# Kernel tuning notes

Hardware: AMD Instinct MI355X
Metric: run time of the kernel (lower is better)

The kernel has to match this reference:

```python
import jax, jax.numpy as jnp
import numpy as np

P = 64       # number of pathways
NV = 512     # features per pathway (nvar[i])
W = 256      # hidden width per pathway
COV = 16     # covariates
B = 2048     # batch
EPS = 1e-5   # BatchNorm eps
SLOPE = 0.2  # LeakyReLU negative slope


def _lrelu(v):
    return jnp.where(v >= 0, v, SLOPE * v)


def setup_inputs() -> dict:
    key = jax.random.key(0)
    ks = jax.random.split(key, 8)
    x = jax.random.normal(ks[0], (B, P * NV + COV), dtype=jnp.float32)
    # per-pathway weights (no bias), stacked across pathways -> grouped GEMM
    W1 = jax.random.normal(ks[1], (P, NV, W), dtype=jnp.float32) * (1.0 / np.sqrt(NV))
    W2 = jax.random.normal(ks[2], (P, W, W), dtype=jnp.float32) * (1.0 / np.sqrt(W))
    W3 = jax.random.normal(ks[3], (P, W), dtype=jnp.float32) * (1.0 / np.sqrt(W))
    gamma = jnp.ones((P,), dtype=jnp.float32)   # bn_path weight
    beta = jnp.zeros((P,), dtype=jnp.float32)   # bn_path bias
    fc_w = jax.random.normal(ks[4], (P + COV, 1), dtype=jnp.float32) * 0.05
    fc_b = jnp.full((1,), 0.001, dtype=jnp.float32)
    return {"x": x, "W1": W1, "W2": W2, "W3": W3,
            "gamma": gamma, "beta": beta, "fc_w": fc_w, "fc_b": fc_b}


def reference(x, W1, W2, W3, gamma, beta, fc_w, fc_b):
    # pathway blocks (dropout = identity in eval): grouped GEMMs over P pathways
    xp = x[:, : P * NV].reshape(B, P, NV)
    h = _lrelu(jnp.einsum('bpi,pio->bpo', xp, W1))
    h = _lrelu(jnp.einsum('bpi,pio->bpo', h, W2))
    p = _lrelu(jnp.einsum('bpi,pi->bp', h, W3))          # [B, P]
    # BatchNorm1d (training-mode batch statistics, biased variance)
    mean = p.mean(axis=0)
    var = p.var(axis=0)
    pn = (p - mean) / jnp.sqrt(var + EPS) * gamma + beta
    # global L2 (Frobenius) normalization, as torch.norm(pathway_layer, 2)
    pn = pn / jnp.linalg.norm(pn)
    # concat covariates, final linear + sigmoid
    z = jnp.concatenate([pn, x[:, P * NV: P * NV + COV]], axis=1)  # [B, P+COV]
    return jax.nn.sigmoid(z @ fc_w + fc_b)                         # [B, 1]
```

## Files before the change

### kernel.cpp

```cpp
#include <hip/hip_runtime.h>
#include <hip/hip_bf16.h>

#define PW 64
#define NV 512
#define HW 256
#define COV 16
#define BATCH 2048
#define XROW (PW * NV + COV)
#define IMG 16384
#define IMG2 8192

typedef short s16x8 __attribute__((ext_vector_type(8)));
typedef float f32x4 __attribute__((ext_vector_type(4)));

__device__ __forceinline__ unsigned short f2bf(float f) {
    union { float f; unsigned int u; } v;
    v.f = f;
    unsigned int u = v.u;
    unsigned int r = (u + 0x7fffu + ((u >> 16) & 1u)) >> 16;
    return (unsigned short)r;
}

__device__ __forceinline__ unsigned int pack2(float a, float b) {
    __hip_bfloat162 h = __float22bfloat162_rn(float2{a, b});
    union { __hip_bfloat162 h; unsigned int u; } c;
    c.h = h;
    return c.u;
}

__device__ __forceinline__ float lrelu(float v) { return v >= 0.f ? v : 0.2f * v; }

__device__ __forceinline__ void gl_lds16(const void* g, void* l) {
    __builtin_amdgcn_global_load_lds(
        (const __attribute__((address_space(1))) void*)g,
        (__attribute__((address_space(3))) void*)l, 16, 0, 0);
}

#define WAITV(n) asm volatile("s_waitcnt vmcnt(" #n ") lgkmcnt(0)" ::: "memory")
#define BAR()    __builtin_amdgcn_s_barrier()
#define SCHED0() __builtin_amdgcn_sched_barrier(0)

__global__ __launch_bounds__(256)
void transpose_all(const float* __restrict__ W1, const float* __restrict__ W2,
                   unsigned short* __restrict__ W1I, unsigned short* __restrict__ W2I) {
    __shared__ float tile[64][260];
    int bx = blockIdx.x;
    const int t = threadIdx.x;
    const bool isW1 = bx < 512;
    const float* src;
    if (isW1) {
        int p = bx >> 3, kb = bx & 7;
        src = W1 + ((size_t)p * NV + kb * 64) * HW;
    } else {
        int b2 = bx - 512;
        int p = b2 >> 2, kb64 = b2 & 3;
        src = W2 + ((size_t)p * HW + kb64 * 64) * HW;
    }
    #pragma unroll
    for (int i = 0; i < 16; ++i) {
        int idx = t + i * 256;
        int r = idx >> 6, c4 = (idx & 63) << 2;
        *(float4*)&tile[r][c4] = *(const float4*)(src + (size_t)r * HW + c4);
    }
    __syncthreads();
    if (isW1) {
        int p = bx >> 3, kb = bx & 7;
        unsigned short* dst = W1I + (size_t)(p * 8 + kb) * IMG;
        #pragma unroll
        for (int pass = 0; pass < 8; ++pass) {
            int idx = pass * 256 + t;
            int n = idx >> 3, s = idx & 7;
            int g = s ^ (n & 7);
            unsigned short v[8];
            #pragma unroll
            for (int j = 0; j < 8; ++j)
                v[j] = f2bf(tile[g * 8 + j][n]);
            *(s16x8*)(dst + (size_t)idx * 8) = *(s16x8*)v;
        }
    } else {
        int b2 = bx - 512;
        int p = b2 >> 2, kb64 = b2 & 3;
        unsigned short* dst = W2I + (size_t)(p * 8 + kb64 * 2) * IMG2;
        #pragma unroll
        for (int pass = 0; pass < 8; ++pass) {
            int idx = pass * 256 + t;
            int h = idx >> 10;
            int rem = idx & 1023;
            int n = rem >> 2, s = rem & 3;
            int g = s ^ ((n >> 1) & 3);
            int krow = h * 32 + g * 8;
            unsigned short v[8];
            #pragma unroll
            for (int j = 0; j < 8; ++j)
                v[j] = f2bf(tile[krow + j][n]);
            *(s16x8*)(dst + (size_t)h * IMG2 + n * 32 + s * 8) = *(s16x8*)v;
        }
    }
}

__global__ __launch_bounds__(512, 2)
void pathway_fused(const float* __restrict__ x, const unsigned short* __restrict__ W1I,
                   const unsigned short* __restrict__ W2I, const float* __restrict__ W3,
                   float* __restrict__ pvec) {
    __shared__ __align__(16) unsigned short lds[81920];

    const int lin = blockIdx.x;
    const int xcd = lin & 7;
    const int idx = lin >> 3;
    const int p   = xcd * 8 + (idx >> 3);
    const int mt  = idx & 7;
    const int bm0 = mt * 256;

    const int t = threadIdx.x;
    const int lane = t & 63;
    const int wave = t >> 6;
    const int wm   = wave >> 2;
    const int wn   = wave & 3;
    const int l15  = lane & 15;
    const int quad = lane >> 4;

    const float* Ap          = x   + (size_t)p * NV;
    const unsigned short* B1 = W1I + (size_t)p * 8 * IMG;
    const unsigned short* B2 = W2I + (size_t)p * 8 * IMG2;

    int arow[8], acolc[8], aoff[8];
    #pragma unroll
    for (int i = 0; i < 8; ++i) {
        int ii = t + i * 512;
        arow[i]  = ii >> 4;
        acolc[i] = (ii & 15) * 4;
        int slot = (acolc[i] >> 3) ^ (arow[i] & 7);
        aoff[i]  = arow[i] * 64 + slot * 8 + (acolc[i] & 7);
    }

    float4 S[8];
    f32x4 acc[8][4] = {};

#define XLOAD(k0) { \
    _Pragma("unroll") \
    for (int i = 0; i < 8; ++i) \
        S[i] = *(const float4*)(Ap + (size_t)(bm0 + arow[i]) * XROW + (k0) + acolc[i]); }

#define APACK(buf) { \
    unsigned short* Asb = lds + (buf) * 16384; \
    _Pragma("unroll") \
    for (int i = 0; i < 8; ++i) { \
        uint2 u; \
        u.x = pack2(S[i].x, S[i].y); \
        u.y = pack2(S[i].z, S[i].w); \
        *(uint2*)&Asb[aoff[i]] = u; } }

#define B1STAGE(buf, kb) { \
    const unsigned short* img = B1 + (size_t)(kb) * IMG; \
    _Pragma("unroll") \
    for (int c = 0; c < 4; ++c) { \
        int off = wave * 4096 + c * 1024; \
        gl_lds16((const char*)img + off + lane * 16, \
                 (char*)lds + 65536 + (buf) * 32768 + off); } }

#define MFMA_A(buf) { \
    const unsigned short* Asb = lds + (buf) * 16384; \
    const unsigned short* Bsb = lds + 32768 + (buf) * 16384; \
    __builtin_amdgcn_s_setprio(1); \
    _Pragma("unroll") \
    for (int kk = 0; kk < 64; kk += 32) { \
        s16x8 af[8], bfr[4]; \
        _Pragma("unroll") \
        for (int mi = 0; mi < 8; ++mi) { \
            int row = wm * 128 + mi * 16 + l15; \
            int slot = ((kk >> 3) + quad) ^ (row & 7); \
            af[mi] = *(const s16x8*)&Asb[row * 64 + slot * 8]; } \
        _Pragma("unroll") \
        for (int ni = 0; ni < 4; ++ni) { \
            int row = wn * 64 + ni * 16 + l15; \
            int slot = ((kk >> 3) + quad) ^ (row & 7); \
            bfr[ni] = *(const s16x8*)&Bsb[row * 64 + slot * 8]; } \
        _Pragma("unroll") \
        for (int mi = 0; mi < 8; ++mi) \
            _Pragma("unroll") \
            for (int ni = 0; ni < 4; ++ni) \
                acc[mi][ni] = __builtin_amdgcn_mfma_f32_16x16x32_bf16( \
                    af[mi], bfr[ni], acc[mi][ni], 0, 0, 0); } \
    __builtin_amdgcn_s_setprio(0); }

#define W2STAGE(buf, kb) { \
    const unsigned short* img = B2 + (size_t)(kb) * IMG2; \
    _Pragma("unroll") \
    for (int c = 0; c < 2; ++c) { \
        int off = wave * 2048 + c * 1024; \
        gl_lds16((const char*)img + off + lane * 16, \
                 (char*)lds + 131072 + (buf) * 16384 + off); } }

#define MFMA_B(buf, kb) { \
    const unsigned short* W2b = lds + 65536 + (buf) * 8192; \
    __builtin_amdgcn_s_setprio(1); \
    { \
        s16x8 af[8], bfr[4]; \
        _Pragma("unroll") \
        for (int mi = 0; mi < 8; ++mi) { \
            int row = wm * 128 + mi * 16 + l15; \
            int slot = ((kb) * 4 + quad) ^ (row & 7); \
            af[mi] = *(const s16x8*)&lds[row * 256 + slot * 8]; } \
        _Pragma("unroll") \
        for (int ni = 0; ni < 4; ++ni) { \
            int row = wn * 64 + ni * 16 + l15; \
            int slot = quad ^ ((row >> 1) & 3); \
            bfr[ni] = *(const s16x8*)&W2b[row * 32 + slot * 8]; } \
        _Pragma("unroll") \
        for (int mi = 0; mi < 8; ++mi) \
            _Pragma("unroll") \
            for (int ni = 0; ni < 4; ++ni) \
                acc[mi][ni] = __builtin_amdgcn_mfma_f32_16x16x32_bf16( \
                    af[mi], bfr[ni], acc[mi][ni], 0, 0, 0); \
    } \
    __builtin_amdgcn_s_setprio(0); }

#define STEP_A(tt, WN) { \
    if ((tt) + 1 < 8) B1STAGE(1 - ((tt) & 1), (tt) + 1); \
    SCHED0(); \
    if ((tt) + 1 < 8) APACK(1 - ((tt) & 1)); \
    if ((tt) + 2 < 8) XLOAD(((tt) + 2) * 64); \
    SCHED0(); \
    MFMA_A((tt) & 1); \
    WAITV(WN); \
    BAR(); \
    SCHED0(); }

#define STEP_B(tt) { \
    if ((tt) + 1 < 8) W2STAGE(1 - ((tt) & 1), (tt) + 1); \
    SCHED0(); \
    MFMA_B((tt) & 1, (tt)); \
    WAITV(0); \
    BAR(); \
    SCHED0(); }

    XLOAD(0);
    SCHED0();
    B1STAGE(0, 0);
    SCHED0();
    APACK(0);
    XLOAD(64);
    WAITV(8);
    BAR();
    SCHED0();

    STEP_A(0, 8);
    STEP_A(1, 8);
    STEP_A(2, 8);
    STEP_A(3, 8);
    STEP_A(4, 8);
    STEP_A(5, 8);
    STEP_A(6, 0);
    STEP_A(7, 0);

    W2STAGE(0, 0);
    SCHED0();
    #pragma unroll
    for (int mi = 0; mi < 8; ++mi)
        #pragma unroll
        for (int ni = 0; ni < 4; ++ni)
            #pragma unroll
            for (int r = 0; r < 4; ++r) {
                int row = wm * 128 + mi * 16 + quad * 4 + r;
                int col = wn * 64 + ni * 16 + l15;
                int slot = (col >> 3) ^ (row & 7);
                lds[row * 256 + slot * 8 + (col & 7)] = f2bf(lrelu(acc[mi][ni][r]));
            }
    WAITV(0);
    BAR();
    SCHED0();

    #pragma unroll
    for (int mi = 0; mi < 8; ++mi)
        #pragma unroll
        for (int ni = 0; ni < 4; ++ni)
            acc[mi][ni] = (f32x4){0.f, 0.f, 0.f, 0.f};

    STEP_B(0);
    STEP_B(1);
    STEP_B(2);
    STEP_B(3);
    STEP_B(4);
    STEP_B(5);
    STEP_B(6);
    STEP_B(7);

    float* red = (float*)lds;
    float w3v[4];
    #pragma unroll
    for (int ni = 0; ni < 4; ++ni)
        w3v[ni] = W3[(size_t)p * HW + wn * 64 + ni * 16 + l15];
    float part[8][4];
    #pragma unroll
    for (int mi = 0; mi < 8; ++mi) {
        #pragma unroll
        for (int r = 0; r < 4; ++r) {
            float s = 0.f;
            #pragma unroll
            for (int ni = 0; ni < 4; ++ni)
                s += lrelu(acc[mi][ni][r]) * w3v[ni];
            part[mi][r] = s;
        }
    }
    #pragma unroll
    for (int off = 1; off < 16; off <<= 1)
        #pragma unroll
        for (int mi = 0; mi < 8; ++mi)
            #pragma unroll
            for (int r = 0; r < 4; ++r)
                part[mi][r] += __shfl_xor(part[mi][r], off);
    if (l15 == 0)
        #pragma unroll
        for (int mi = 0; mi < 8; ++mi)
            #pragma unroll
            for (int r = 0; r < 4; ++r)
                red[wn * 256 + wm * 128 + mi * 16 + quad * 4 + r] = part[mi][r];
    __syncthreads();
    if (t < 256) {
        float s = red[0 * 256 + t] + red[1 * 256 + t] + red[2 * 256 + t] + red[3 * 256 + t];
        pvec[(size_t)p * BATCH + bm0 + t] = lrelu(s);
    }
#undef XLOAD
#undef APACK
#undef B1STAGE
#undef MFMA_A
#undef W2STAGE
#undef MFMA_B
#undef STEP_A
#undef STEP_B
}

__global__ __launch_bounds__(256)
void stats_k(const float* __restrict__ pvec, float* __restrict__ stat) {
    const int p = blockIdx.x;
    float s = 0.f, q = 0.f;
    for (int i = threadIdx.x; i < BATCH; i += 256) {
        float v = pvec[(size_t)p * BATCH + i];
        s += v; q += v * v;
    }
    #pragma unroll
    for (int off = 32; off; off >>= 1) {
        s += __shfl_down(s, off);
        q += __shfl_down(q, off);
    }
    __shared__ float ls[4], lq[4];
    const int wave = threadIdx.x >> 6, lane = threadIdx.x & 63;
    if (lane == 0) { ls[wave] = s; lq[wave] = q; }
    __syncthreads();
    if (threadIdx.x == 0) {
        float S = ls[0] + ls[1] + ls[2] + ls[3];
        float Q = lq[0] + lq[1] + lq[2] + lq[3];
        float mean = S * (1.f / BATCH);
        float var  = Q * (1.f / BATCH) - mean * mean;
        stat[p]       = mean;
        stat[64 + p]  = rsqrtf(var + 1e-5f);
        stat[128 + p] = var;
    }
}

__global__ __launch_bounds__(256)
void final_k(const float* __restrict__ pvec, const float* __restrict__ stat,
             const float* __restrict__ gamma, const float* __restrict__ beta,
             const float* __restrict__ x, const float* __restrict__ fc_w,
             const float* __restrict__ fc_b, float* __restrict__ out) {
    const int b = blockIdx.x * 256 + threadIdx.x;
    float nsq = 0.f;
    #pragma unroll
    for (int p = 0; p < PW; ++p) {
        float g = gamma[p], bt = beta[p], var = stat[128 + p], inv = stat[64 + p];
        nsq += (float)BATCH * (g * g * var * inv * inv + bt * bt);
    }
    const float rn = rsqrtf(nsq);
    float acc = fc_b[0];
    #pragma unroll
    for (int p = 0; p < PW; ++p) {
        float pn = (pvec[(size_t)p * BATCH + b] - stat[p]) * stat[64 + p] * gamma[p] + beta[p];
        acc += pn * rn * fc_w[p];
    }
    #pragma unroll
    for (int c = 0; c < COV; ++c)
        acc += x[(size_t)b * XROW + PW * NV + c] * fc_w[PW + c];
    out[b] = 1.f / (1.f + __expf(-acc));
}

extern "C" void kernel_launch(void* const* d_in, const int* in_sizes, int n_in,
                              void* d_out, int out_size, void* d_ws, size_t ws_size,
                              hipStream_t stream) {
    const float* x     = (const float*)d_in[0];
    const float* W1    = (const float*)d_in[1];
    const float* W2    = (const float*)d_in[2];
    const float* W3    = (const float*)d_in[3];
    const float* gamma = (const float*)d_in[4];
    const float* beta  = (const float*)d_in[5];
    const float* fc_w  = (const float*)d_in[6];
    const float* fc_b  = (const float*)d_in[7];
    float* out = (float*)d_out;

    char* ws = (char*)d_ws;
    size_t off = 0;
    unsigned short* W1I = (unsigned short*)(ws + off); off += (size_t)PW * NV * HW * 2;
    unsigned short* W2I = (unsigned short*)(ws + off); off += (size_t)PW * HW * HW * 2;
    float* pvec = (float*)(ws + off); off += (size_t)PW * BATCH * 4;
    float* stat = (float*)(ws + off); off += 256 * 4;

    transpose_all<<<dim3(512 + 256), 256, 0, stream>>>(W1, W2, W1I, W2I);
    pathway_fused<<<dim3(512), 512, 0, stream>>>(x, W1I, W2I, W3, pvec);
    stats_k<<<PW, 256, 0, stream>>>(pvec, stat);
    final_k<<<BATCH / 256, 256, 0, stream>>>(pvec, stat, gamma, beta, x, fc_w, fc_b, out);
}
```

Baseline: 455.8 us.

## Triple-buffer W1 staging in GEMM1 and fuse batch statistics into pathway kernel

Reworks the first GEMM loop so W1 tiles are staged into three LDS buffers two steps ahead, and moves the X pack after the MFMA block so loads overlap compute more deeply. It also folds the per-pathway sum and sum-of-squares reduction into the fused kernel's epilogue using atomics. This removes the separate stats kernel launch and its re-read of pvec. The atomics are zeroed inside the transpose kernel, which adds a dependency, and float atomic ordering makes the statistics nondeterministic.

```diff
diff --git a/kernel.cpp b/kernel.cpp
--- a/kernel.cpp
+++ b/kernel.cpp
@@ -42,10 +42,12 @@
 
 __global__ __launch_bounds__(256)
 void transpose_all(const float* __restrict__ W1, const float* __restrict__ W2,
-                   unsigned short* __restrict__ W1I, unsigned short* __restrict__ W2I) {
+                   unsigned short* __restrict__ W1I, unsigned short* __restrict__ W2I,
+                   float* __restrict__ accbuf) {
     __shared__ float tile[64][260];
     int bx = blockIdx.x;
     const int t = threadIdx.x;
+    if (bx == 0 && t < 128) accbuf[t] = 0.f;
     const bool isW1 = bx < 512;
     const float* src;
     if (isW1) {
@@ -101,7 +103,7 @@
 __global__ __launch_bounds__(512, 2)
 void pathway_fused(const float* __restrict__ x, const unsigned short* __restrict__ W1I,
                    const unsigned short* __restrict__ W2I, const float* __restrict__ W3,
-                   float* __restrict__ pvec) {
+                   float* __restrict__ pvec, float* __restrict__ accbuf) {
     __shared__ __align__(16) unsigned short lds[81920];
 
     const int lin = blockIdx.x;
@@ -142,7 +144,7 @@
         S[i] = *(const float4*)(Ap + (size_t)(bm0 + arow[i]) * XROW + (k0) + acolc[i]); }
 
 #define APACK(buf) { \
-    unsigned short* Asb = lds + (buf) * 16384; \
+    unsigned short* Asb = lds + 49152 + (buf) * 16384; \
     _Pragma("unroll") \
     for (int i = 0; i < 8; ++i) { \
         uint2 u; \
@@ -156,11 +158,11 @@
     for (int c = 0; c < 4; ++c) { \
         int off = wave * 4096 + c * 1024; \
         gl_lds16((const char*)img + off + lane * 16, \
-                 (char*)lds + 65536 + (buf) * 32768 + off); } }
-
-#define MFMA_A(buf) { \
-    const unsigned short* Asb = lds + (buf) * 16384; \
-    const unsigned short* Bsb = lds + 32768 + (buf) * 16384; \
+                 (char*)lds + (buf) * 32768 + off); } }
+
+#define MFMA_A(abuf, bbuf) { \
+    const unsigned short* Asb = lds + 49152 + (abuf) * 16384; \
+    const unsigned short* Bsb = lds + (bbuf) * 16384; \
     __builtin_amdgcn_s_setprio(1); \
     _Pragma("unroll") \
     for (int kk = 0; kk < 64; kk += 32) { \
@@ -215,14 +217,14 @@
     } \
     __builtin_amdgcn_s_setprio(0); }
 
-#define STEP_A(tt, WN) { \
-    if ((tt) + 1 < 8) B1STAGE(1 - ((tt) & 1), (tt) + 1); \
+#define STEP_A_MAIN(SB, SKB, AB, BB, PB, LK) { \
+    B1STAGE(SB, SKB); \
     SCHED0(); \
-    if ((tt) + 1 < 8) APACK(1 - ((tt) & 1)); \
-    if ((tt) + 2 < 8) XLOAD(((tt) + 2) * 64); \
+    MFMA_A(AB, BB); \
     SCHED0(); \
-    MFMA_A((tt) & 1); \
-    WAITV(WN); \
+    APACK(PB); \
+    XLOAD(LK); \
+    WAITV(12); \
     BAR(); \
     SCHED0(); }
 
@@ -237,21 +239,34 @@
     XLOAD(0);
     SCHED0();
     B1STAGE(0, 0);
+    B1STAGE(1, 1);
     SCHED0();
     APACK(0);
     XLOAD(64);
-    WAITV(8);
+    WAITV(12);
     BAR();
     SCHED0();
 
-    STEP_A(0, 8);
-    STEP_A(1, 8);
-    STEP_A(2, 8);
-    STEP_A(3, 8);
-    STEP_A(4, 8);
-    STEP_A(5, 8);
-    STEP_A(6, 0);
-    STEP_A(7, 0);
+    STEP_A_MAIN(2, 2, 0, 0, 1, 128);
+    STEP_A_MAIN(0, 3, 1, 1, 0, 192);
+    STEP_A_MAIN(1, 4, 0, 2, 1, 256);
+    STEP_A_MAIN(2, 5, 1, 0, 0, 320);
+    STEP_A_MAIN(0, 6, 0, 1, 1, 384);
+    STEP_A_MAIN(1, 7, 1, 2, 0, 448);
+    {
+        MFMA_A(0, 0);
+        SCHED0();
+        APACK(1);
+        WAITV(0);
+        BAR();
+        SCHED0();
+    }
+    {
+        MFMA_A(1, 1);
+        WAITV(0);
+        BAR();
+        SCHED0();
+    }
 
     W2STAGE(0, 0);
     SCHED0();
@@ -286,6 +301,7 @@
     STEP_B(7);
 
     float* red = (float*)lds;
+    float* lsq = (float*)lds + 1024;
     float w3v[4];
     #pragma unroll
     for (int ni = 0; ni < 4; ++ni)
@@ -318,7 +334,20 @@
     __syncthreads();
     if (t < 256) {
         float s = red[0 * 256 + t] + red[1 * 256 + t] + red[2 * 256 + t] + red[3 * 256 + t];
-        pvec[(size_t)p * BATCH + bm0 + t] = lrelu(s);
+        float v = lrelu(s);
+        pvec[(size_t)p * BATCH + bm0 + t] = v;
+        float sq = v * v;
+        #pragma unroll
+        for (int off = 32; off; off >>= 1) {
+            v  += __shfl_down(v, off);
+            sq += __shfl_down(sq, off);
+        }
+        if (lane == 0) { lsq[wave] = v; lsq[4 + wave] = sq; }
+    }
+    __syncthreads();
+    if (t == 0) {
+        atomicAdd(accbuf + p,      lsq[0] + lsq[1] + lsq[2] + lsq[3]);
+        atomicAdd(accbuf + 64 + p, lsq[4] + lsq[5] + lsq[6] + lsq[7]);
     }
 #undef XLOAD
 #undef APACK
@@ -326,55 +355,33 @@
 #undef MFMA_A
 #undef W2STAGE
 #undef MFMA_B
-#undef STEP_A
+#undef STEP_A_MAIN
 #undef STEP_B
 }
 
 __global__ __launch_bounds__(256)
-void stats_k(const float* __restrict__ pvec, float* __restrict__ stat) {
-    const int p = blockIdx.x;
-    float s = 0.f, q = 0.f;
-    for (int i = threadIdx.x; i < BATCH; i += 256) {
-        float v = pvec[(size_t)p * BATCH + i];
-        s += v; q += v * v;
-    }
-    #pragma unroll
-    for (int off = 32; off; off >>= 1) {
-        s += __shfl_down(s, off);
-        q += __shfl_down(q, off);
-    }
-    __shared__ float ls[4], lq[4];
-    const int wave = threadIdx.x >> 6, lane = threadIdx.x & 63;
-    if (lane == 0) { ls[wave] = s; lq[wave] = q; }
-    __syncthreads();
-    if (threadIdx.x == 0) {
-        float S = ls[0] + ls[1] + ls[2] + ls[3];
-        float Q = lq[0] + lq[1] + lq[2] + lq[3];
-        float mean = S * (1.f / BATCH);
-        float var  = Q * (1.f / BATCH) - mean * mean;
-        stat[p]       = mean;
-        stat[64 + p]  = rsqrtf(var + 1e-5f);
-        stat[128 + p] = var;
-    }
-}
-
-__global__ __launch_bounds__(256)
-void final_k(const float* __restrict__ pvec, const float* __restrict__ stat,
+void final_k(const float* __restrict__ pvec, const float* __restrict__ accbuf,
              const float* __restrict__ gamma, const float* __restrict__ beta,
              const float* __restrict__ x, const float* __restrict__ fc_w,
              const float* __restrict__ fc_b, float* __restrict__ out) {
     const int b = blockIdx.x * 256 + threadIdx.x;
+    const float invB = 1.f / BATCH;
+    float mean_[PW], inv_[PW];
     float nsq = 0.f;
     #pragma unroll
     for (int p = 0; p < PW; ++p) {
-        float g = gamma[p], bt = beta[p], var = stat[128 + p], inv = stat[64 + p];
+        float mean = accbuf[p] * invB;
+        float var  = accbuf[64 + p] * invB - mean * mean;
+        float inv  = rsqrtf(var + 1e-5f);
+        mean_[p] = mean; inv_[p] = inv;
+        float g = gamma[p], bt = beta[p];
         nsq += (float)BATCH * (g * g * var * inv * inv + bt * bt);
     }
     const float rn = rsqrtf(nsq);
     float acc = fc_b[0];
     #pragma unroll
     for (int p = 0; p < PW; ++p) {
-        float pn = (pvec[(size_t)p * BATCH + b] - stat[p]) * stat[64 + p] * gamma[p] + beta[p];
+        float pn = (pvec[(size_t)p * BATCH + b] - mean_[p]) * inv_[p] * gamma[p] + beta[p];
         acc += pn * rn * fc_w[p];
     }
     #pragma unroll
@@ -401,10 +408,9 @@
     unsigned short* W1I = (unsigned short*)(ws + off); off += (size_t)PW * NV * HW * 2;
     unsigned short* W2I = (unsigned short*)(ws + off); off += (size_t)PW * HW * HW * 2;
     float* pvec = (float*)(ws + off); off += (size_t)PW * BATCH * 4;
-    float* stat = (float*)(ws + off); off += 256 * 4;
-
-    transpose_all<<<dim3(512 + 256), 256, 0, stream>>>(W1, W2, W1I, W2I);
-    pathway_fused<<<dim3(512), 512, 0, stream>>>(x, W1I, W2I, W3, pvec);
-    stats_k<<<PW, 256, 0, stream>>>(pvec, stat);
-    final_k<<<BATCH / 256, 256, 0, stream>>>(pvec, stat, gamma, beta, x, fc_w, fc_b, out);
-}
+    float* accbuf = (float*)(ws + off); off += 256 * 4;
+
+    transpose_all<<<dim3(512 + 256), 256, 0, stream>>>(W1, W2, W1I, W2I, accbuf);
+    pathway_fused<<<dim3(512), 512, 0, stream>>>(x, W1I, W2I, W3, pvec, accbuf);
+    final_k<<<BATCH / 256, 256, 0, stream>>>(pvec, accbuf, gamma, beta, x, fc_w, fc_b, out);
+}
```

New measurement: 469.5 us. +3.0%, slower.
